# Optimization experiments

Measured on AMD Instinct MI355X. Metric: run time of the kernel, lower is better.

## Reference

```python
import jax, jax.numpy as jnp
import numpy as np

N_NODES = 100000
N_EDGES = 1600000


def _add_self_loops(edge_index, num_nodes):
    loop = jnp.arange(num_nodes, dtype=edge_index.dtype)
    src = jnp.concatenate([edge_index[0], loop])
    dst = jnp.concatenate([edge_index[1], loop])
    return src, dst


def _gcn_conv(x, src, dst, W, b, num_nodes):
    # PyG GCNConv: h = x W, then symmetric-normalized scatter-add aggregation.
    h = x @ W  # [N, F_out]
    ones = jnp.ones(src.shape[0], dtype=x.dtype)
    deg = jax.ops.segment_sum(ones, dst, num_segments=num_nodes)  # in-degree incl. self-loops
    dinv = jnp.where(deg > 0, jax.lax.rsqrt(deg), 0.0)
    norm = dinv[src] * dinv[dst]  # [E]
    msg = h[src] * norm[:, None]  # irregular gather, [E, F_out]
    out = jax.ops.segment_sum(msg, dst, num_segments=num_nodes)  # scatter-add, [N, F_out]
    return out + b


def setup_inputs() -> dict:
    key = jax.random.key(0)
    ks = jax.random.split(key, 4)
    x = jax.random.uniform(ks[0], (N_NODES, 32), dtype=jnp.float32)
    edge_index = jax.random.randint(ks[1], (2, N_EDGES), 0, N_NODES, dtype=jnp.int64)
    W1 = jax.random.normal(ks[2], (32, 64), dtype=jnp.float32) * (1.0 / np.sqrt(32))
    b1 = jnp.zeros((64,), dtype=jnp.float32)
    W2 = jax.random.normal(ks[3], (64, 128), dtype=jnp.float32) * (1.0 / np.sqrt(64))
    b2 = jnp.zeros((128,), dtype=jnp.float32)
    return {"x": x, "edge_index": edge_index, "W1": W1, "b1": b1, "W2": W2, "b2": b2}


def reference(x, edge_index, W1, b1, W2, b2):
    num_nodes = x.shape[0]
    src, dst = _add_self_loops(edge_index, num_nodes)
    h = _gcn_conv(x, src, dst, W1, b1, num_nodes)
    h = jax.nn.relu(h)
    out = _gcn_conv(h, src, dst, W2, b2, num_nodes)
    return out
```

## Files before the change

kernel.cpp:

```cpp
#include <hip/hip_runtime.h>
#include <hip/hip_fp16.h>

static inline int cdiv(int a, int b) { return (a + b - 1) / b; }

#define BK_SHIFT 8
#define NBLK2 1024
#define SCAN_BS 1024
#define MAXB 6144

struct h2x4 { __half2 a, b, c, d; };

__global__ __launch_bounds__(256) void kb1(const int* __restrict__ dst, int E, int epb, int nbuk,
                                           int* __restrict__ cnt) {
    __shared__ int h[512];
    int blk = blockIdx.x;
    for (int b = threadIdx.x; b < nbuk; b += 256) h[b] = 0;
    __syncthreads();
    int beg = blk * epb, end = min(E, beg + epb);
    for (int e = beg + threadIdx.x; e < end; e += 256)
        atomicAdd(&h[dst[e] >> BK_SHIFT], 1);
    __syncthreads();
    for (int b = threadIdx.x; b < nbuk; b += 256) cnt[(size_t)b * NBLK2 + blk] = h[b];
}

__global__ __launch_bounds__(SCAN_BS) void k_blocksum(const int* __restrict__ v, int n, int* __restrict__ bsum) {
    __shared__ int s[SCAN_BS];
    int t = threadIdx.x;
    int i = blockIdx.x * SCAN_BS + t;
    s[t] = (i < n) ? v[i] : 0;
    __syncthreads();
    for (int off = SCAN_BS / 2; off > 0; off >>= 1) {
        if (t < off) s[t] += s[t + off];
        __syncthreads();
    }
    if (t == 0) bsum[blockIdx.x] = s[0];
}

__global__ __launch_bounds__(512) void k_scan_bsums(const int* __restrict__ bsum, int NB, int* __restrict__ boff) {
    __shared__ int s[512];
    int t = threadIdx.x;
    int v = (t < NB) ? bsum[t] : 0;
    s[t] = v;
    __syncthreads();
    for (int off = 1; off < 512; off <<= 1) {
        int u = (t >= off) ? s[t - off] : 0;
        __syncthreads();
        s[t] += u;
        __syncthreads();
    }
    if (t < NB) boff[t] = s[t] - v;
}

__global__ __launch_bounds__(SCAN_BS) void k_scan_final(const int* __restrict__ v, int n,
                                                        const int* __restrict__ boff,
                                                        int* __restrict__ outp, int E) {
    __shared__ int s[SCAN_BS];
    int t = threadIdx.x;
    int i = blockIdx.x * SCAN_BS + t;
    int x = (i < n) ? v[i] : 0;
    s[t] = x;
    __syncthreads();
    for (int off = 1; off < SCAN_BS; off <<= 1) {
        int u = (t >= off) ? s[t - off] : 0;
        __syncthreads();
        s[t] += u;
        __syncthreads();
    }
    if (i < n) outp[i] = boff[blockIdx.x] + s[t] - x;
    if (blockIdx.x == 0 && t == 0) outp[n] = E;
}

__global__ __launch_bounds__(256) void kb2(const int* __restrict__ ei, int E, int epb, int nbuk,
                                           const int* __restrict__ cbase,
                                           unsigned int* __restrict__ pairs) {
    __shared__ int lb[512];
    int blk = blockIdx.x;
    for (int b = threadIdx.x; b < nbuk; b += 256) lb[b] = cbase[(size_t)b * NBLK2 + blk];
    __syncthreads();
    int beg = blk * epb, end = min(E, beg + epb);
    const int* dst = ei + E;
    for (int e = beg + threadIdx.x; e < end; e += 256) {
        int d = dst[e];
        int s = ei[e];
        int slot = atomicAdd(&lb[d >> BK_SHIFT], 1);
        pairs[slot] = (unsigned)s | ((unsigned)(d & 255) << 17);
    }
}

__global__ __launch_bounds__(1024) void k_sortbucket(const unsigned int* __restrict__ pairs,
                                                     const int* __restrict__ cbase, int nbuk, int N, int E,
                                                     int* __restrict__ csr_src,
                                                     int* __restrict__ offsets,
                                                     float* __restrict__ dinv) {
    __shared__ int c[256];
    __shared__ int ex[256];
    __shared__ int sorted[MAXB];
    int b = blockIdx.x;
    int tid = threadIdx.x;
    int base = cbase[(size_t)b * NBLK2];
    int endp = cbase[(size_t)(b + 1) * NBLK2];
    int n = endp - base;
    if (tid < 256) c[tid] = 0;
    __syncthreads();
    int sr_[6], dl_[6], rk_[6];
#pragma unroll
    for (int k = 0; k < 6; ++k) {
        int i = tid + k * 1024;
        if (i < n) {
            unsigned int p = pairs[base + i];
            sr_[k] = (int)(p & 0x1FFFFu);
            dl_[k] = (int)(p >> 17);
            rk_[k] = atomicAdd(&c[dl_[k]], 1);
        }
    }
    __syncthreads();
    if (tid < 256) ex[tid] = c[tid];
    __syncthreads();
    for (int off = 1; off < 256; off <<= 1) {
        int u = (tid >= off && tid < 256) ? ex[tid - off] : 0;
        __syncthreads();
        if (tid < 256) ex[tid] += u;
        __syncthreads();
    }
    if (tid < 256) ex[tid] -= c[tid];
    __syncthreads();
#pragma unroll
    for (int k = 0; k < 6; ++k) {
        int i = tid + k * 1024;
        if (i < n) sorted[ex[dl_[k]] + rk_[k]] = sr_[k];
    }
    __syncthreads();
    for (int i = tid; i < n; i += 1024) csr_src[base + i] = sorted[i];
    if (tid < 256) {
        int g = (b << BK_SHIFT) + tid;
        if (g < N) {
            offsets[g] = base + ex[tid];
            dinv[g] = rsqrtf((float)(c[tid] + 1));
        }
    }
    if (b == 0 && tid == 0) offsets[N] = E;
}

__global__ __launch_bounds__(256) void k_cast32(const float* __restrict__ x, const float* __restrict__ dinv,
                                                __half* __restrict__ xh, int N) {
    int i = blockIdx.x * 256 + threadIdx.x;
    if (i >= N * 8) return;
    int g = i >> 3;
    float di = dinv[g];
    float4 v = ((const float4*)x)[i];
    __half2 h0 = __floats2half2_rn(v.x * di, v.y * di);
    __half2 h1 = __floats2half2_rn(v.z * di, v.w * di);
    ((__half2*)xh)[2 * i] = h0;
    ((__half2*)xh)[2 * i + 1] = h1;
}

__global__ __launch_bounds__(512) void k_fused1(const __half* __restrict__ feat,
                                                const int* __restrict__ offsets,
                                                const int* __restrict__ csr_src,
                                                const float* __restrict__ dinv,
                                                const float* __restrict__ W,
                                                const float* __restrict__ b,
                                                __half* __restrict__ out, int N) {
    __shared__ float sX[128][33];
    __shared__ float sW[32][64];
    __shared__ float sDi[128];
    int tid = threadIdx.x;
    int g0 = blockIdx.x * 128;

    {
        const float4* Wv = (const float4*)W;
        float4* sWv = (float4*)&sW[0][0];
        sWv[tid] = Wv[tid];
    }
    {
        int gl = tid >> 2, q = tid & 3;
        int g = g0 + gl;
        const h2x4* f8 = (const h2x4*)feat;
        float acc[8] = {0.f, 0.f, 0.f, 0.f, 0.f, 0.f, 0.f, 0.f};
        float di = 0.f;
        if (g < N) {
            di = dinv[g];
            h2x4 w = f8[(size_t)g * 4 + q];
            float2 u;
            u = __half22float2(w.a); acc[0] = u.x; acc[1] = u.y;
            u = __half22float2(w.b); acc[2] = u.x; acc[3] = u.y;
            u = __half22float2(w.c); acc[4] = u.x; acc[5] = u.y;
            u = __half22float2(w.d); acc[6] = u.x; acc[7] = u.y;
            int beg = offsets[g], end = offsets[g + 1];
            int e = beg;
            for (; e + 4 <= end; e += 4) {
                int s0 = csr_src[e + 0], s1 = csr_src[e + 1], s2 = csr_src[e + 2], s3 = csr_src[e + 3];
                h2x4 w0 = f8[(size_t)s0 * 4 + q];
                h2x4 w1 = f8[(size_t)s1 * 4 + q];
                h2x4 w2 = f8[(size_t)s2 * 4 + q];
                h2x4 w3 = f8[(size_t)s3 * 4 + q];
                u = __half22float2(w0.a); acc[0] += u.x; acc[1] += u.y;
                u = __half22float2(w0.b); acc[2] += u.x; acc[3] += u.y;
                u = __half22float2(w0.c); acc[4] += u.x; acc[5] += u.y;
                u = __half22float2(w0.d); acc[6] += u.x; acc[7] += u.y;
                u = __half22float2(w1.a); acc[0] += u.x; acc[1] += u.y;
                u = __half22float2(w1.b); acc[2] += u.x; acc[3] += u.y;
                u = __half22float2(w1.c); acc[4] += u.x; acc[5] += u.y;
                u = __half22float2(w1.d); acc[6] += u.x; acc[7] += u.y;
                u = __half22float2(w2.a); acc[0] += u.x; acc[1] += u.y;
                u = __half22float2(w2.b); acc[2] += u.x; acc[3] += u.y;
                u = __half22float2(w2.c); acc[4] += u.x; acc[5] += u.y;
                u = __half22float2(w2.d); acc[6] += u.x; acc[7] += u.y;
                u = __half22float2(w3.a); acc[0] += u.x; acc[1] += u.y;
                u = __half22float2(w3.b); acc[2] += u.x; acc[3] += u.y;
                u = __half22float2(w3.c); acc[4] += u.x; acc[5] += u.y;
                u = __half22float2(w3.d); acc[6] += u.x; acc[7] += u.y;
            }
            for (; e < end; ++e) {
                h2x4 w4 = f8[(size_t)csr_src[e] * 4 + q];
                u = __half22float2(w4.a); acc[0] += u.x; acc[1] += u.y;
                u = __half22float2(w4.b); acc[2] += u.x; acc[3] += u.y;
                u = __half22float2(w4.c); acc[4] += u.x; acc[5] += u.y;
                u = __half22float2(w4.d); acc[6] += u.x; acc[7] += u.y;
            }
        }
        if (q == 0) sDi[gl] = di;
#pragma unroll
        for (int j = 0; j < 8; ++j) sX[gl][q * 8 + j] = acc[j] * di;
    }
    __syncthreads();
    int tm = tid & 31, tn = tid >> 5;
    float acc2[4][4];
    {
        float4 bb = *(const float4*)(b + tn * 4);
#pragma unroll
        for (int i = 0; i < 4; ++i) {
            acc2[i][0] = bb.x; acc2[i][1] = bb.y; acc2[i][2] = bb.z; acc2[i][3] = bb.w;
        }
    }
#pragma unroll 4
    for (int k = 0; k < 32; ++k) {
        float a0 = sX[tm * 4 + 0][k];
        float a1 = sX[tm * 4 + 1][k];
        float a2 = sX[tm * 4 + 2][k];
        float a3 = sX[tm * 4 + 3][k];
        float4 w = *(const float4*)&sW[k][tn * 4];
        float wv[4] = {w.x, w.y, w.z, w.w};
#pragma unroll
        for (int j = 0; j < 4; ++j) {
            acc2[0][j] = fmaf(a0, wv[j], acc2[0][j]);
            acc2[1][j] = fmaf(a1, wv[j], acc2[1][j]);
            acc2[2][j] = fmaf(a2, wv[j], acc2[2][j]);
            acc2[3][j] = fmaf(a3, wv[j], acc2[3][j]);
        }
    }
#pragma unroll
    for (int i = 0; i < 4; ++i) {
        int row = g0 + tm * 4 + i;
        if (row < N) {
            float di = sDi[tm * 4 + i];
            __half2 p0 = __floats2half2_rn(fmaxf(acc2[i][0], 0.f) * di, fmaxf(acc2[i][1], 0.f) * di);
            __half2 p1 = __floats2half2_rn(fmaxf(acc2[i][2], 0.f) * di, fmaxf(acc2[i][3], 0.f) * di);
            __half2* op = (__half2*)(out + (size_t)row * 64);
            op[tn * 2] = p0;
            op[tn * 2 + 1] = p1;
        }
    }
}

__global__ __launch_bounds__(512) void k_fused2(const __half* __restrict__ feat,
                                                const int* __restrict__ offsets,
                                                const int* __restrict__ csr_src,
                                                const float* __restrict__ dinv,
                                                const float* __restrict__ W,
                                                const float* __restrict__ b,
                                                float* __restrict__ out, int N) {
    __shared__ float sX[64][69];
    __shared__ float sW[64][128];
    int tid = threadIdx.x;
    int g0 = blockIdx.x * 64;

    {
        const float4* Wv = (const float4*)W;
        float4* sWv = (float4*)&sW[0][0];
#pragma unroll
        for (int i = 0; i < 4; ++i) sWv[tid + 512 * i] = Wv[tid + 512 * i];
    }
    {
        int gl = tid >> 3, q = tid & 7;
        int g = g0 + gl;
        const h2x4* f8 = (const h2x4*)feat;
        float acc[8] = {0.f, 0.f, 0.f, 0.f, 0.f, 0.f, 0.f, 0.f};
        float di = 0.f;
        if (g < N) {
            di = dinv[g];
            h2x4 w = f8[(size_t)g * 8 + q];
            float2 u;
            u = __half22float2(w.a); acc[0] = u.x; acc[1] = u.y;
            u = __half22float2(w.b); acc[2] = u.x; acc[3] = u.y;
            u = __half22float2(w.c); acc[4] = u.x; acc[5] = u.y;
            u = __half22float2(w.d); acc[6] = u.x; acc[7] = u.y;
            int beg = offsets[g], end = offsets[g + 1];
            int e = beg;
            for (; e + 4 <= end; e += 4) {
                int s0 = csr_src[e + 0], s1 = csr_src[e + 1], s2 = csr_src[e + 2], s3 = csr_src[e + 3];
                h2x4 w0 = f8[(size_t)s0 * 8 + q];
                h2x4 w1 = f8[(size_t)s1 * 8 + q];
                h2x4 w2 = f8[(size_t)s2 * 8 + q];
                h2x4 w3 = f8[(size_t)s3 * 8 + q];
                u = __half22float2(w0.a); acc[0] += u.x; acc[1] += u.y;
                u = __half22float2(w0.b); acc[2] += u.x; acc[3] += u.y;
                u = __half22float2(w0.c); acc[4] += u.x; acc[5] += u.y;
                u = __half22float2(w0.d); acc[6] += u.x; acc[7] += u.y;
                u = __half22float2(w1.a); acc[0] += u.x; acc[1] += u.y;
                u = __half22float2(w1.b); acc[2] += u.x; acc[3] += u.y;
                u = __half22float2(w1.c); acc[4] += u.x; acc[5] += u.y;
                u = __half22float2(w1.d); acc[6] += u.x; acc[7] += u.y;
                u = __half22float2(w2.a); acc[0] += u.x; acc[1] += u.y;
                u = __half22float2(w2.b); acc[2] += u.x; acc[3] += u.y;
                u = __half22float2(w2.c); acc[4] += u.x; acc[5] += u.y;
                u = __half22float2(w2.d); acc[6] += u.x; acc[7] += u.y;
                u = __half22float2(w3.a); acc[0] += u.x; acc[1] += u.y;
                u = __half22float2(w3.b); acc[2] += u.x; acc[3] += u.y;
                u = __half22float2(w3.c); acc[4] += u.x; acc[5] += u.y;
                u = __half22float2(w3.d); acc[6] += u.x; acc[7] += u.y;
            }
            for (; e < end; ++e) {
                h2x4 w4 = f8[(size_t)csr_src[e] * 8 + q];
                u = __half22float2(w4.a); acc[0] += u.x; acc[1] += u.y;
                u = __half22float2(w4.b); acc[2] += u.x; acc[3] += u.y;
                u = __half22float2(w4.c); acc[4] += u.x; acc[5] += u.y;
                u = __half22float2(w4.d); acc[6] += u.x; acc[7] += u.y;
            }
        }
#pragma unroll
        for (int j = 0; j < 8; ++j) sX[gl][q * 8 + j] = acc[j] * di;
    }
    __syncthreads();
    int tm = tid & 15, tn = tid >> 4;
    float acc2[4][4];
    {
        float4 bb = *(const float4*)(b + tn * 4);
#pragma unroll
        for (int i = 0; i < 4; ++i) {
            acc2[i][0] = bb.x; acc2[i][1] = bb.y; acc2[i][2] = bb.z; acc2[i][3] = bb.w;
        }
    }
#pragma unroll 4
    for (int k = 0; k < 64; ++k) {
        float a0 = sX[tm * 4 + 0][k];
        float a1 = sX[tm * 4 + 1][k];
        float a2 = sX[tm * 4 + 2][k];
        float a3 = sX[tm * 4 + 3][k];
        float4 w = *(const float4*)&sW[k][tn * 4];
        float wv[4] = {w.x, w.y, w.z, w.w};
#pragma unroll
        for (int j = 0; j < 4; ++j) {
            acc2[0][j] = fmaf(a0, wv[j], acc2[0][j]);
            acc2[1][j] = fmaf(a1, wv[j], acc2[1][j]);
            acc2[2][j] = fmaf(a2, wv[j], acc2[2][j]);
            acc2[3][j] = fmaf(a3, wv[j], acc2[3][j]);
        }
    }
#pragma unroll
    for (int i = 0; i < 4; ++i) {
        int row = g0 + tm * 4 + i;
        if (row < N) {
            *(float4*)(out + (size_t)row * 128 + tn * 4) =
                make_float4(acc2[i][0], acc2[i][1], acc2[i][2], acc2[i][3]);
        }
    }
}

extern "C" void kernel_launch(void* const* d_in, const int* in_sizes, int n_in,
                              void* d_out, int out_size, void* d_ws, size_t ws_size,
                              hipStream_t stream) {
    const float* x  = (const float*)d_in[0];
    const int*   ei = (const int*)d_in[1];
    const float* W1 = (const float*)d_in[2];
    const float* b1 = (const float*)d_in[3];
    const float* W2 = (const float*)d_in[4];
    const float* b2 = (const float*)d_in[5];
    float* out = (float*)d_out;

    const int N = in_sizes[0] / 32;
    const int E = in_sizes[1] / 2;
    const int epb = cdiv(E, NBLK2);
    const int nbuk = cdiv(N, 1 << BK_SHIFT);
    const int clen = nbuk * NBLK2;

    char* ws = (char*)d_ws;
    size_t off = 0;
    auto walloc = [&](size_t bytes) -> void* {
        void* p = ws + off;
        off = (off + bytes + 255) & ~(size_t)255;
        return p;
    };
    int*          cnt     = (int*)          walloc((size_t)(clen + 4) * 4);
    int*          cbase   = (int*)          walloc((size_t)(clen + 4) * 4);
    int*          bsum    = (int*)          walloc(512 * 4);
    int*          boff    = (int*)          walloc(512 * 4);
    unsigned int* pairs   = (unsigned int*) walloc((size_t)E * 4);
    int*          csr_src = (int*)          walloc((size_t)E * 4);
    int*          offsets = (int*)          walloc((size_t)(N + 4) * 4);
    float*        dinv    = (float*)        walloc((size_t)N * 4);
    __half*       xh      = (__half*)       walloc((size_t)N * 32 * 2);
    __half*       h2h     = (__half*)       walloc((size_t)N * 64 * 2);
    (void)ws_size; (void)n_in; (void)out_size;

    kb1<<<NBLK2, 256, 0, stream>>>(ei + E, E, epb, nbuk, cnt);

    const int NB = cdiv(clen, SCAN_BS);
    k_blocksum<<<NB, SCAN_BS, 0, stream>>>(cnt, clen, bsum);
    k_scan_bsums<<<1, 512, 0, stream>>>(bsum, NB, boff);
    k_scan_final<<<NB, SCAN_BS, 0, stream>>>(cnt, clen, boff, cbase, E);

    kb2<<<NBLK2, 256, 0, stream>>>(ei, E, epb, nbuk, cbase, pairs);
    k_sortbucket<<<nbuk, 1024, 0, stream>>>(pairs, cbase, nbuk, N, E, csr_src, offsets, dinv);

    k_cast32<<<cdiv(N * 8, 256), 256, 0, stream>>>(x, dinv, xh, N);

    k_fused1<<<cdiv(N, 128), 512, 0, stream>>>(xh, offsets, csr_src, dinv, W1, b1, h2h, N);
    k_fused2<<<cdiv(N, 64), 512, 0, stream>>>(h2h, offsets, csr_src, dinv, W2, b2, out, N);
}
```

Before: 147.6 us.

## Split layer-2 fused aggregate+GEMM into separate aggregation and GEMM kernels

Replaces the fused layer-2 kernel with two kernels: a lightweight gather-aggregate kernel (256 threads, no shared memory) that writes a float32 intermediate, followed by a tiled GEMM with a 4x8 register tile and transposed A in shared memory. The aim is to give the irregular gather higher occupancy, since it no longer carries the large shared-memory footprint of the GEMM, and to make the GEMM more efficient. The cost is an extra launch plus a 25.6 MB float32 intermediate that must be written and read back.

```diff
diff --git a/kernel.cpp b/kernel.cpp
--- a/kernel.cpp
+++ b/kernel.cpp
@@ -263,106 +263,128 @@
     }
 }
 
-__global__ __launch_bounds__(512) void k_fused2(const __half* __restrict__ feat,
-                                                const int* __restrict__ offsets,
-                                                const int* __restrict__ csr_src,
-                                                const float* __restrict__ dinv,
-                                                const float* __restrict__ W,
-                                                const float* __restrict__ b,
-                                                float* __restrict__ out, int N) {
-    __shared__ float sX[64][69];
+__global__ __launch_bounds__(256) void k_agg64(const __half* __restrict__ feat,
+                                               const int* __restrict__ offsets,
+                                               const int* __restrict__ csr_src,
+                                               const float* __restrict__ dinv,
+                                               float* __restrict__ out, int N) {
+    constexpr int L = 8;
+    int t = blockIdx.x * 256 + threadIdx.x;
+    int g = t / L;
+    int q = t % L;
+    if (g >= N) return;
+    const h2x4* f8 = (const h2x4*)feat;
+    int beg = offsets[g];
+    int end = offsets[g + 1];
+    float di = dinv[g];
+    float acc[8];
+    {
+        h2x4 w = f8[(size_t)g * L + q];
+        float2 p0 = __half22float2(w.a), p1 = __half22float2(w.b);
+        float2 p2 = __half22float2(w.c), p3 = __half22float2(w.d);
+        acc[0] = p0.x; acc[1] = p0.y; acc[2] = p1.x; acc[3] = p1.y;
+        acc[4] = p2.x; acc[5] = p2.y; acc[6] = p3.x; acc[7] = p3.y;
+    }
+    int e = beg;
+    for (; e + 4 <= end; e += 4) {
+        int s0 = csr_src[e + 0], s1 = csr_src[e + 1], s2 = csr_src[e + 2], s3 = csr_src[e + 3];
+        h2x4 w0 = f8[(size_t)s0 * L + q];
+        h2x4 w1 = f8[(size_t)s1 * L + q];
+        h2x4 w2 = f8[(size_t)s2 * L + q];
+        h2x4 w3 = f8[(size_t)s3 * L + q];
+        float2 u;
+        u = __half22float2(w0.a); acc[0] += u.x; acc[1] += u.y;
+        u = __half22float2(w0.b); acc[2] += u.x; acc[3] += u.y;
+        u = __half22float2(w0.c); acc[4] += u.x; acc[5] += u.y;
+        u = __half22float2(w0.d); acc[6] += u.x; acc[7] += u.y;
+        u = __half22float2(w1.a); acc[0] += u.x; acc[1] += u.y;
+        u = __half22float2(w1.b); acc[2] += u.x; acc[3] += u.y;
+        u = __half22float2(w1.c); acc[4] += u.x; acc[5] += u.y;
+        u = __half22float2(w1.d); acc[6] += u.x; acc[7] += u.y;
+        u = __half22float2(w2.a); acc[0] += u.x; acc[1] += u.y;
+        u = __half22float2(w2.b); acc[2] += u.x; acc[3] += u.y;
+        u = __half22float2(w2.c); acc[4] += u.x; acc[5] += u.y;
+        u = __half22float2(w2.d); acc[6] += u.x; acc[7] += u.y;
+        u = __half22float2(w3.a); acc[0] += u.x; acc[1] += u.y;
+        u = __half22float2(w3.b); acc[2] += u.x; acc[3] += u.y;
+        u = __half22float2(w3.c); acc[4] += u.x; acc[5] += u.y;
+        u = __half22float2(w3.d); acc[6] += u.x; acc[7] += u.y;
+    }
+    for (; e < end; ++e) {
+        h2x4 w = f8[(size_t)csr_src[e] * L + q];
+        float2 u;
+        u = __half22float2(w.a); acc[0] += u.x; acc[1] += u.y;
+        u = __half22float2(w.b); acc[2] += u.x; acc[3] += u.y;
+        u = __half22float2(w.c); acc[4] += u.x; acc[5] += u.y;
+        u = __half22float2(w.d); acc[6] += u.x; acc[7] += u.y;
+    }
+    float4 o0 = make_float4(acc[0] * di, acc[1] * di, acc[2] * di, acc[3] * di);
+    float4 o1 = make_float4(acc[4] * di, acc[5] * di, acc[6] * di, acc[7] * di);
+    ((float4*)out)[(size_t)g * 16 + q * 2] = o0;
+    ((float4*)out)[(size_t)g * 16 + q * 2 + 1] = o1;
+}
+
+__global__ __launch_bounds__(256) void k_gemm2(const float* __restrict__ A, const float* __restrict__ W,
+                                               const float* __restrict__ b, float* __restrict__ out, int N) {
+    __shared__ float sA[64][68];
     __shared__ float sW[64][128];
     int tid = threadIdx.x;
-    int g0 = blockIdx.x * 64;
+    int row0 = blockIdx.x * 64;
 
     {
         const float4* Wv = (const float4*)W;
         float4* sWv = (float4*)&sW[0][0];
 #pragma unroll
-        for (int i = 0; i < 4; ++i) sWv[tid + 512 * i] = Wv[tid + 512 * i];
-    }
-    {
-        int gl = tid >> 3, q = tid & 7;
-        int g = g0 + gl;
-        const h2x4* f8 = (const h2x4*)feat;
-        float acc[8] = {0.f, 0.f, 0.f, 0.f, 0.f, 0.f, 0.f, 0.f};
-        float di = 0.f;
-        if (g < N) {
-            di = dinv[g];
-            h2x4 w = f8[(size_t)g * 8 + q];
-            float2 u;
-            u = __half22float2(w.a); acc[0] = u.x; acc[1] = u.y;
-            u = __half22float2(w.b); acc[2] = u.x; acc[3] = u.y;
-            u = __half22float2(w.c); acc[4] = u.x; acc[5] = u.y;
-            u = __half22float2(w.d); acc[6] = u.x; acc[7] = u.y;
-            int beg = offsets[g], end = offsets[g + 1];
-            int e = beg;
-            for (; e + 4 <= end; e += 4) {
-                int s0 = csr_src[e + 0], s1 = csr_src[e + 1], s2 = csr_src[e + 2], s3 = csr_src[e + 3];
-                h2x4 w0 = f8[(size_t)s0 * 8 + q];
-                h2x4 w1 = f8[(size_t)s1 * 8 + q];
-                h2x4 w2 = f8[(size_t)s2 * 8 + q];
-                h2x4 w3 = f8[(size_t)s3 * 8 + q];
-                u = __half22float2(w0.a); acc[0] += u.x; acc[1] += u.y;
-                u = __half22float2(w0.b); acc[2] += u.x; acc[3] += u.y;
-                u = __half22float2(w0.c); acc[4] += u.x; acc[5] += u.y;
-                u = __half22float2(w0.d); acc[6] += u.x; acc[7] += u.y;
-                u = __half22float2(w1.a); acc[0] += u.x; acc[1] += u.y;
-                u = __half22float2(w1.b); acc[2] += u.x; acc[3] += u.y;
-                u = __half22float2(w1.c); acc[4] += u.x; acc[5] += u.y;
-                u = __half22float2(w1.d); acc[6] += u.x; acc[7] += u.y;
-                u = __half22float2(w2.a); acc[0] += u.x; acc[1] += u.y;
-                u = __half22float2(w2.b); acc[2] += u.x; acc[3] += u.y;
-                u = __half22float2(w2.c); acc[4] += u.x; acc[5] += u.y;
-                u = __half22float2(w2.d); acc[6] += u.x; acc[7] += u.y;
-                u = __half22float2(w3.a); acc[0] += u.x; acc[1] += u.y;
-                u = __half22float2(w3.b); acc[2] += u.x; acc[3] += u.y;
-                u = __half22float2(w3.c); acc[4] += u.x; acc[5] += u.y;
-                u = __half22float2(w3.d); acc[6] += u.x; acc[7] += u.y;
-            }
-            for (; e < end; ++e) {
-                h2x4 w4 = f8[(size_t)csr_src[e] * 8 + q];
-                u = __half22float2(w4.a); acc[0] += u.x; acc[1] += u.y;
-                u = __half22float2(w4.b); acc[2] += u.x; acc[3] += u.y;
-                u = __half22float2(w4.c); acc[4] += u.x; acc[5] += u.y;
-                u = __half22float2(w4.d); acc[6] += u.x; acc[7] += u.y;
-            }
-        }
-#pragma unroll
-        for (int j = 0; j < 8; ++j) sX[gl][q * 8 + j] = acc[j] * di;
-    }
-    __syncthreads();
+        for (int i = 0; i < 8; ++i) sWv[tid + 256 * i] = Wv[tid + 256 * i];
+    }
+    {
+        int row = tid >> 2;
+        int gr = row0 + row;
+        int kq = (tid & 3) * 4;
+#pragma unroll
+        for (int i = 0; i < 4; ++i) {
+            int k0 = kq + 16 * i;
+            float4 v = (gr < N) ? *(const float4*)(A + (size_t)gr * 64 + k0)
+                                : make_float4(0.f, 0.f, 0.f, 0.f);
+            sA[k0 + 0][row] = v.x;
+            sA[k0 + 1][row] = v.y;
+            sA[k0 + 2][row] = v.z;
+            sA[k0 + 3][row] = v.w;
+        }
+    }
+    __syncthreads();
+
     int tm = tid & 15, tn = tid >> 4;
-    float acc2[4][4];
-    {
-        float4 bb = *(const float4*)(b + tn * 4);
+    float acc[4][8];
+    {
+        float4 b0 = *(const float4*)(b + tn * 8);
+        float4 b1 = *(const float4*)(b + tn * 8 + 4);
 #pragma unroll
         for (int i = 0; i < 4; ++i) {
-            acc2[i][0] = bb.x; acc2[i][1] = bb.y; acc2[i][2] = bb.z; acc2[i][3] = bb.w;
+            acc[i][0] = b0.x; acc[i][1] = b0.y; acc[i][2] = b0.z; acc[i][3] = b0.w;
+            acc[i][4] = b1.x; acc[i][5] = b1.y; acc[i][6] = b1.z; acc[i][7] = b1.w;
         }
     }
 #pragma unroll 4
     for (int k = 0; k < 64; ++k) {
-        float a0 = sX[tm * 4 + 0][k];
-        float a1 = sX[tm * 4 + 1][k];
-        float a2 = sX[tm * 4 + 2][k];
-        float a3 = sX[tm * 4 + 3][k];
-        float4 w = *(const float4*)&sW[k][tn * 4];
-        float wv[4] = {w.x, w.y, w.z, w.w};
-#pragma unroll
-        for (int j = 0; j < 4; ++j) {
-            acc2[0][j] = fmaf(a0, wv[j], acc2[0][j]);
-            acc2[1][j] = fmaf(a1, wv[j], acc2[1][j]);
-            acc2[2][j] = fmaf(a2, wv[j], acc2[2][j]);
-            acc2[3][j] = fmaf(a3, wv[j], acc2[3][j]);
-        }
+        float4 a = *(const float4*)&sA[k][tm * 4];
+        float4 w0 = *(const float4*)&sW[k][tn * 8];
+        float4 w1 = *(const float4*)&sW[k][tn * 8 + 4];
+        float av[4] = {a.x, a.y, a.z, a.w};
+        float wv[8] = {w0.x, w0.y, w0.z, w0.w, w1.x, w1.y, w1.z, w1.w};
+#pragma unroll
+        for (int i = 0; i < 4; ++i)
+#pragma unroll
+            for (int j = 0; j < 8; ++j) acc[i][j] = fmaf(av[i], wv[j], acc[i][j]);
     }
 #pragma unroll
     for (int i = 0; i < 4; ++i) {
-        int row = g0 + tm * 4 + i;
+        int row = row0 + tm * 4 + i;
         if (row < N) {
-            *(float4*)(out + (size_t)row * 128 + tn * 4) =
-                make_float4(acc2[i][0], acc2[i][1], acc2[i][2], acc2[i][3]);
+            *(float4*)(out + (size_t)row * 128 + tn * 8) =
+                make_float4(acc[i][0], acc[i][1], acc[i][2], acc[i][3]);
+            *(float4*)(out + (size_t)row * 128 + tn * 8 + 4) =
+                make_float4(acc[i][4], acc[i][5], acc[i][6], acc[i][7]);
         }
     }
 }
@@ -401,6 +423,7 @@
     float*        dinv    = (float*)        walloc((size_t)N * 4);
     __half*       xh      = (__half*)       walloc((size_t)N * 32 * 2);
     __half*       h2h     = (__half*)       walloc((size_t)N * 64 * 2);
+    float*        a2      = (float*)        walloc((size_t)N * 64 * 4);
     (void)ws_size; (void)n_in; (void)out_size;
 
     kb1<<<NBLK2, 256, 0, stream>>>(ei + E, E, epb, nbuk, cnt);
@@ -416,5 +439,7 @@
     k_cast32<<<cdiv(N * 8, 256), 256, 0, stream>>>(x, dinv, xh, N);
 
     k_fused1<<<cdiv(N, 128), 512, 0, stream>>>(xh, offsets, csr_src, dinv, W1, b1, h2h, N);
-    k_fused2<<<cdiv(N, 64), 512, 0, stream>>>(h2h, offsets, csr_src, dinv, W2, b2, out, N);
-}
+
+    k_agg64<<<cdiv(N * 8, 256), 256, 0, stream>>>(h2h, offsets, csr_src, dinv, a2, N);
+    k_gemm2<<<cdiv(N, 64), 256, 0, stream>>>(a2, W2, b2, out, N);
+}
```

Measured after the change: 149.5 us. No clear change (+1.3%).
